# Kernel optimization log

Measured on AMD Instinct MI355X. Metric: run time of the kernel, lower is better.

## Reference

```python
import jax, jax.numpy as jnp
import numpy as np

# Correlation layer constants (match init_kwargs / torch defaults)
MAX_DISP = 20      # max_displacement
STRIDE2 = 2
KERNEL = 3         # kernel_size (only used in the normalization)
D = 2 * MAX_DISP + 1  # 41 displacement steps per axis


def setup_inputs() -> dict:
    key = jax.random.key(0)
    k1, k2 = jax.random.split(key)
    b, c, h, w = 4, 64, 96, 160
    input1 = jax.random.normal(k1, (b, c, h, w), dtype=jnp.float32)
    input2 = jax.random.normal(k2, (b, c, h, w), dtype=jnp.float32)
    return {"input1": input1, "input2": input2}


def _correlation(input1, input2):
    b, c, h, w = input1.shape
    # displacement offsets: (i - max_displacement//2) * stride2, i in [0, D)
    offs = (jnp.arange(D) - MAX_DISP // 2) * STRIDE2  # ranges -20 .. +60
    # output channel m = i*D + j uses dx = offs[i] (W shift), dy = offs[j] (H shift)
    dxs = jnp.repeat(offs, D)  # [D*D]
    dys = jnp.tile(offs, D)    # [D*D]
    P = int((D - 1 - MAX_DISP // 2) * STRIDE2)  # = 60, max |shift|
    padded = jnp.pad(input2, ((0, 0), (0, 0), (P, P), (P, P)))
    # shifted[..., y, x] = input2[..., y - dy, x - dx] (zero outside)
    def step(carry, disp):
        dy, dx = disp
        sl = jax.lax.dynamic_slice(padded, (0, 0, P - dy, P - dx), (b, c, h, w))
        return carry, (input1 * sl).sum(axis=1)  # [b, h, w]
    _, out = jax.lax.scan(step, None, (dys, dxs))  # [D*D, b, h, w]
    out = jnp.transpose(out, (1, 0, 2, 3))  # [b, D*D, h, w]
    return out / (c * KERNEL * KERNEL)


def reference(input1, input2):
    return _correlation(input1, input2)
```

## Files before the change

kernel.cpp:

```cpp
#include <hip/hip_runtime.h>
#include <hip/hip_bf16.h>


#define B_ 4
#define C_ 64
#define H_ 96
#define W_ 160
#define DD 41
#define HW_ (H_*W_)
#define RS 72
#define GS 161

typedef __bf16 bf16x8 __attribute__((ext_vector_type(8)));
typedef float  f32x4  __attribute__((ext_vector_type(4)));

__global__ void to_nhwc(const float* __restrict__ s1, const float* __restrict__ s2,
                        ushort* __restrict__ d1, ushort* __restrict__ d2) {
    int p = blockIdx.x * 256 + threadIdx.x;
    const float* src = blockIdx.y ? s2 : s1;
    ushort* dst = blockIdx.y ? d2 : d1;
    int b = p / HW_;
    int rem = p - b * HW_;
    const float* sp = src + (size_t)b * (C_ * HW_) + rem;
    ushort tmp[C_];
#pragma unroll
    for (int c = 0; c < C_; ++c) {
        union { float f; unsigned u; } uu;
        uu.f = sp[(size_t)c * HW_];
        unsigned r = uu.u + 0x7FFF + ((uu.u >> 16) & 1);
        tmp[c] = (ushort)(r >> 16);
    }
    uint4* dp = (uint4*)(dst + (size_t)p * C_);
#pragma unroll
    for (int k = 0; k < 8; ++k) dp[k] = ((uint4*)tmp)[k];
}

__global__ __launch_bounds__(256) void corr_kernel(const ushort* __restrict__ in1w,
                                                   const ushort* __restrict__ in2w,
                                                   float* __restrict__ out) {
    __shared__ ushort s2[2 * 80 * RS];
    __shared__ float  gd[DD * GS];

    const int j   = blockIdx.x;
    const int y   = blockIdx.y;
    const int b   = blockIdx.z;
    const int tid = threadIdx.x;
    const int lane = tid & 63;
    const int w    = tid >> 6;
    const int y2 = y + 20 - 2 * j;
    const bool valid_row = (y2 >= 0) && (y2 < H_);

    if (valid_row) {
        const uint4* src = (const uint4*)(in2w + (size_t)((b * H_ + y2) * W_) * C_);
#pragma unroll
        for (int it = 0; it < 5; ++it) {
            int cidx = it * 256 + tid;
            int u  = cidx >> 3;
            int co = (cidx & 7) * 8;
            uint4 v = src[cidx];
            *(uint4*)&s2[((u & 1) * 80 + (u >> 1)) * RS + co] = v;
        }
        __syncthreads();

        const int quad = lane >> 4;
        const int l15  = lane & 15;
        const ushort* a_base = in1w + (size_t)((b * H_ + y) * W_) * C_;
        for (int t = 0; t < 10; ++t) {
            int p  = w * 10 + t;
            int mi = p >> 2;
            int nt = p & 3;
            int par = (mi >= 5) ? 1 : 0;
            int x0  = (mi - 5 * par) * 32;
            int xa = x0 + par + 2 * l15;
            const bf16x8* aptr = (const bf16x8*)(const void*)(a_base + xa * C_ + quad * 8);
            bf16x8 a0 = aptr[0];
            bf16x8 a1 = aptr[4];
            int u0 = x0 + par - 60 + 32 * nt;
            int u  = u0 + 2 * l15;
            bf16x8 b0 = {}, b1 = {};
            if (u >= 0 && u < W_) {
                const bf16x8* bptr =
                    (const bf16x8*)(const void*)&s2[((u & 1) * 80 + (u >> 1)) * RS + quad * 8];
                b0 = bptr[0];
                b1 = bptr[4];
            }
            f32x4 acc = {};
            acc = __builtin_amdgcn_mfma_f32_16x16x32_bf16(a0, b0, acc, 0, 0, 0);
            acc = __builtin_amdgcn_mfma_f32_16x16x32_bf16(a1, b1, acc, 0, 0, 0);
#pragma unroll
            for (int r = 0; r < 4; ++r) {
                int mx = quad * 4 + r;
                int i  = mx - l15 - 16 * nt + 40;
                if (i >= 0 && i <= 40) {
                    int x = x0 + par + 2 * mx;
                    gd[i * GS + x] = acc[r];
                }
            }
        }
        __syncthreads();
    }

    const float scale = 1.0f / 576.0f;
    for (int i = w; i < DD; i += 4) {
        float* op = out + ((size_t)(b * (DD * DD) + i * DD + j) * H_ + y) * W_;
        if (valid_row) {
            op[lane]       = gd[i * GS + lane] * scale;
            op[lane + 64]  = gd[i * GS + lane + 64] * scale;
            if (lane < 32) op[lane + 128] = gd[i * GS + lane + 128] * scale;
        } else {
            op[lane]      = 0.0f;
            op[lane + 64] = 0.0f;
            if (lane < 32) op[lane + 128] = 0.0f;
        }
    }
}

extern "C" void kernel_launch(void* const* d_in, const int* in_sizes, int n_in,
                              void* d_out, int out_size, void* d_ws, size_t ws_size,
                              hipStream_t stream) {
    const float* in1 = (const float*)d_in[0];
    const float* in2 = (const float*)d_in[1];
    float* out = (float*)d_out;
    ushort* w1 = (ushort*)d_ws;
    ushort* w2 = w1 + (size_t)B_ * H_ * W_ * C_;
    to_nhwc<<<dim3((B_ * HW_) / 256, 2), 256, 0, stream>>>(in1, in2, w1, w2);
    corr_kernel<<<dim3(DD, H_, B_), 256, 0, stream>>>(w1, w2, out);
}
```

Measured before the change: 531.7 us.

## Swap grid axes, use nontemporal output stores, pack bf16 pairs in conversion

Three separate changes. The grid now launches y on x and j on y, so consecutive blocks handle adjacent rows for the same vertical displacement; this is meant to improve how output writes and input-row reads line up in cache. Output stores become nontemporal so the large write-only output does not pollute cache. The NHWC conversion packs two bf16 values into each 32-bit word instead of building a ushort array, which should simplify register handling.

```diff
diff --git a/kernel.cpp b/kernel.cpp
--- a/kernel.cpp
+++ b/kernel.cpp
@@ -13,6 +13,7 @@
 
 typedef __bf16 bf16x8 __attribute__((ext_vector_type(8)));
 typedef float  f32x4  __attribute__((ext_vector_type(4)));
+typedef unsigned int u32x4 __attribute__((ext_vector_type(4)));
 
 __global__ void to_nhwc(const float* __restrict__ s1, const float* __restrict__ s2,
                         ushort* __restrict__ d1, ushort* __restrict__ d2) {
@@ -22,17 +23,22 @@
     int b = p / HW_;
     int rem = p - b * HW_;
     const float* sp = src + (size_t)b * (C_ * HW_) + rem;
-    ushort tmp[C_];
+    unsigned words[32];
 #pragma unroll
-    for (int c = 0; c < C_; ++c) {
-        union { float f; unsigned u; } uu;
-        uu.f = sp[(size_t)c * HW_];
-        unsigned r = uu.u + 0x7FFF + ((uu.u >> 16) & 1);
-        tmp[c] = (ushort)(r >> 16);
+    for (int k = 0; k < 32; ++k) {
+        union { float f; unsigned u; } lo, hi;
+        lo.f = sp[(size_t)(2 * k) * HW_];
+        hi.f = sp[(size_t)(2 * k + 1) * HW_];
+        unsigned rl = (lo.u + 0x7FFFu + ((lo.u >> 16) & 1u)) >> 16;
+        unsigned rh = (hi.u + 0x7FFFu + ((hi.u >> 16) & 1u)) & 0xFFFF0000u;
+        words[k] = rl | rh;
     }
-    uint4* dp = (uint4*)(dst + (size_t)p * C_);
+    u32x4* dp = (u32x4*)(dst + (size_t)p * C_);
 #pragma unroll
-    for (int k = 0; k < 8; ++k) dp[k] = ((uint4*)tmp)[k];
+    for (int k = 0; k < 8; ++k) {
+        u32x4 v = { words[4 * k], words[4 * k + 1], words[4 * k + 2], words[4 * k + 3] };
+        dp[k] = v;
+    }
 }
 
 __global__ __launch_bounds__(256) void corr_kernel(const ushort* __restrict__ in1w,
@@ -41,8 +47,8 @@
     __shared__ ushort s2[2 * 80 * RS];
     __shared__ float  gd[DD * GS];
 
-    const int j   = blockIdx.x;
-    const int y   = blockIdx.y;
+    const int y   = blockIdx.x;
+    const int j   = blockIdx.y;
     const int b   = blockIdx.z;
     const int tid = threadIdx.x;
     const int lane = tid & 63;
@@ -104,13 +110,15 @@
     for (int i = w; i < DD; i += 4) {
         float* op = out + ((size_t)(b * (DD * DD) + i * DD + j) * H_ + y) * W_;
         if (valid_row) {
-            op[lane]       = gd[i * GS + lane] * scale;
-            op[lane + 64]  = gd[i * GS + lane + 64] * scale;
-            if (lane < 32) op[lane + 128] = gd[i * GS + lane + 128] * scale;
+            __builtin_nontemporal_store(gd[i * GS + lane] * scale, op + lane);
+            __builtin_nontemporal_store(gd[i * GS + lane + 64] * scale, op + lane + 64);
+            if (lane < 32)
+                __builtin_nontemporal_store(gd[i * GS + lane + 128] * scale, op + lane + 128);
         } else {
-            op[lane]      = 0.0f;
-            op[lane + 64] = 0.0f;
-            if (lane < 32) op[lane + 128] = 0.0f;
+            __builtin_nontemporal_store(0.0f, op + lane);
+            __builtin_nontemporal_store(0.0f, op + lane + 64);
+            if (lane < 32)
+                __builtin_nontemporal_store(0.0f, op + lane + 128);
         }
     }
 }
@@ -124,5 +132,5 @@
     ushort* w1 = (ushort*)d_ws;
     ushort* w2 = w1 + (size_t)B_ * H_ * W_ * C_;
     to_nhwc<<<dim3((B_ * HW_) / 256, 2), 256, 0, stream>>>(in1, in2, w1, w2);
-    corr_kernel<<<dim3(DD, H_, B_), 256, 0, stream>>>(w1, w2, out);
+    corr_kernel<<<dim3(H_, DD, B_), 256, 0, stream>>>(w1, w2, out);
 }
```

After: 494.4 us. -7.0%, faster.
